# Performance work log

Hardware: AMD Instinct MI355X
Metric: run time of the kernel (lower is better)

## Reference

```python
import jax, jax.numpy as jnp
import numpy as np
import itertools

N_GRAPHS = 64
NODES_PER_GRAPH = 16
N_NODES = N_GRAPHS * NODES_PER_GRAPH  # 1024


def conv2d(x, w, b, stride=1):
    # x: [N, Cin, H, W], w: [Cout, Cin, 3, 3], padding=1 (same as torch Conv2d(...,3,stride,1))
    y = jax.lax.conv_general_dilated(
        x, w, (stride, stride), ((1, 1), (1, 1)),
        dimension_numbers=("NCHW", "OIHW", "NCHW"))
    return y + b[None, :, None, None]


def lrelu(x):
    return jax.nn.leaky_relu(x, 0.1)


def conv_mpn(x, edges, c1w, c1b, c2w, c2b, c3w, c3b):
    # ConvMPN: gather neighbour / non-neighbour node features, scatter_add to dst,
    # concat on channel dim, then 3 convs (no activation in between, as in source).
    n = x.shape[0]
    a, s, b = edges[:, 0], edges[:, 1], edges[:, 2]
    src = jnp.concatenate([a, b])  # bidirectional, matches torch cat([e0,e2]) / cat([e2,e0])
    dst = jnp.concatenate([b, a])
    pos = jnp.concatenate([s > 0, s > 0]).astype(x.dtype)
    neg = jnp.concatenate([s < 0, s < 0]).astype(x.dtype)
    gathered = x[src]  # [2E, C, H, W]
    neigh = jax.ops.segment_sum(gathered * pos[:, None, None, None], dst, num_segments=n)
    non = jax.ops.segment_sum(gathered * neg[:, None, None, None], dst, num_segments=n)
    h = jnp.concatenate([x, neigh, non], axis=1)  # [N, 3C, H, W]
    h = conv2d(h, c1w, c1b)
    h = conv2d(h, c2w, c2b)
    h = conv2d(h, c3w, c3b)
    return h


def setup_inputs() -> dict:
    key = jax.random.key(0)
    ks = iter(jax.random.split(key, 40))

    def p(shape):
        fan_in = int(np.prod(shape[1:])) if len(shape) > 1 else shape[0]
        return jax.random.normal(next(ks), shape, dtype=jnp.float32) / np.sqrt(fan_in)

    x = jax.random.normal(next(ks), (N_NODES, 32, 32), dtype=jnp.float32)
    t = jax.random.normal(next(ks), (N_NODES, 10), dtype=jnp.float32)

    # complete graph per sample; sign +/-1 marks neighbour vs non-neighbour
    pairs = np.array(list(itertools.combinations(range(NODES_PER_GRAPH), 2)))  # (120, 2)
    offs = np.arange(N_GRAPHS)[:, None] * NODES_PER_GRAPH
    aa = (pairs[None, :, 0] + offs).ravel()
    bb = (pairs[None, :, 1] + offs).ravel()
    rng = np.random.RandomState(0)
    sign = rng.choice(np.array([-1, 1]), size=aa.shape[0])
    edges = jnp.asarray(np.stack([aa, sign, bb], axis=1).astype(np.int64))
    nd_to_sample = jnp.asarray(np.repeat(np.arange(N_GRAPHS), NODES_PER_GRAPH).astype(np.int64))

    inp = {
        "x": x, "t": t, "edges": edges, "nd_to_sample": nd_to_sample,
        "w_t": p((8192, 10)), "b_t": jnp.zeros((8192,), jnp.float32),
        "c1w": p((16, 9, 3, 3)), "c1b": jnp.zeros((16,), jnp.float32),
        "c2w": p((16, 16, 3, 3)), "c2b": jnp.zeros((16,), jnp.float32),
        "c3w": p((16, 16, 3, 3)), "c3b": jnp.zeros((16,), jnp.float32),
        "m1c1w": p((32, 48, 3, 3)), "m1c1b": jnp.zeros((32,), jnp.float32),
        "m1c2w": p((32, 32, 3, 3)), "m1c2b": jnp.zeros((32,), jnp.float32),
        "m1c3w": p((16, 32, 3, 3)), "m1c3b": jnp.zeros((16,), jnp.float32),
        "ds1w": p((16, 16, 3, 3)), "ds1b": jnp.zeros((16,), jnp.float32),
        "m2c1w": p((32, 48, 3, 3)), "m2c1b": jnp.zeros((32,), jnp.float32),
        "m2c2w": p((32, 32, 3, 3)), "m2c2b": jnp.zeros((32,), jnp.float32),
        "m2c3w": p((16, 32, 3, 3)), "m2c3b": jnp.zeros((16,), jnp.float32),
        "ds2w": p((16, 16, 3, 3)), "ds2b": jnp.zeros((16,), jnp.float32),
        "d1w": p((256, 16, 3, 3)), "d1b": jnp.zeros((256,), jnp.float32),
        "d2w": p((128, 256, 3, 3)), "d2b": jnp.zeros((128,), jnp.float32),
        "d3w": p((128, 128, 3, 3)), "d3b": jnp.zeros((128,), jnp.float32),
        "pw": p((1, 128)), "pb": jnp.zeros((1,), jnp.float32),
    }
    return inp


def reference(x, t, edges, nd_to_sample,
              w_t, b_t, c1w, c1b, c2w, c2b, c3w, c3b,
              m1c1w, m1c1b, m1c2w, m1c2b, m1c3w, m1c3b, ds1w, ds1b,
              m2c1w, m2c1b, m2c2w, m2c2b, m2c3w, m2c3b, ds2w, ds2b,
              d1w, d1b, d2w, d2b, d3w, d3b, pw, pb):
    h = x.reshape(-1, 1, 32, 32)
    tt = (t @ w_t.T + b_t).reshape(-1, 8, 32, 32)
    h = jnp.concatenate([h, tt], axis=1)  # [N, 9, 32, 32]
    h = lrelu(conv2d(h, c1w, c1b))
    h = lrelu(conv2d(h, c2w, c2b))
    h = lrelu(conv2d(h, c3w, c3b))
    h = conv_mpn(h, edges, m1c1w, m1c1b, m1c2w, m1c2b, m1c3w, m1c3b)
    h = lrelu(conv2d(h, ds1w, ds1b, stride=2))  # 32 -> 16
    h = conv_mpn(h, edges, m2c1w, m2c1b, m2c2w, m2c2b, m2c3w, m2c3b)
    h = lrelu(conv2d(h, ds2w, ds2b, stride=2))  # 16 -> 8
    h = lrelu(conv2d(h, d1w, d1b, stride=2))    # 8 -> 4
    h = lrelu(conv2d(h, d2w, d2b, stride=2))    # 4 -> 2
    h = lrelu(conv2d(h, d3w, d3b, stride=2))    # 2 -> 1
    h = h.reshape(-1, h.shape[1])               # [N, 128]
    pooled = jax.ops.segment_sum(h, nd_to_sample, num_segments=N_GRAPHS)  # add_pool
    return pooled @ pw.T + pb                    # [B, 1]
```

## Files before the change

kernel.cpp:

```cpp
#include <hip/hip_runtime.h>
#include <hip/hip_bf16.h>


#define N_NODES   1024
#define N_GRAPHS  64

typedef __hip_bfloat16 bf16;
typedef __attribute__((ext_vector_type(8)))  short  short8;
typedef __attribute__((ext_vector_type(16))) float  f32x16;

__device__ __forceinline__ float bf2f(unsigned short s) {
    union { unsigned u; float f; } x; x.u = ((unsigned)s) << 16; return x.f;
}
__device__ __forceinline__ unsigned short f2bf(float f) {
    __hip_bfloat16 h = __float2bfloat16(f);
    return *reinterpret_cast<unsigned short*>(&h);
}
__device__ __forceinline__ uint4 pack8(const float* f) {
    uint4 r;
    r.x = f2bf(f[0]) | ((unsigned)f2bf(f[1]) << 16);
    r.y = f2bf(f[2]) | ((unsigned)f2bf(f[3]) << 16);
    r.z = f2bf(f[4]) | ((unsigned)f2bf(f[5]) << 16);
    r.w = f2bf(f[6]) | ((unsigned)f2bf(f[7]) << 16);
    return r;
}

template<int N>
__device__ __forceinline__ void zacc(f32x16* a) {
    #pragma unroll
    for (int i = 0; i < N; ++i)
        #pragma unroll
        for (int e = 0; e < 16; ++e) a[i][e] = 0.f;
}

template<int TPW, int NW>
__device__ __forceinline__ void mfma_rr32(
    const short* lds, int inbase, int zch,
    const unsigned short* wfb, int kkstride_sh,
    f32x16* acc, int wid, int lane)
{
    const int pxl = lane & 31, kg = lane >> 5;
    short8 wfr[9];
    #pragma unroll
    for (int kk = 0; kk < 9; ++kk)
        wfr[kk] = *(const short8*)(wfb + (size_t)kk * kkstride_sh + lane * 8);
    const int r0 = wid * TPW;
    #pragma unroll
    for (int ir = 0; ir < TPW + 2; ++ir) {
        int iy = r0 - 1 + ir;
        if (iy < 0 || iy > 31) continue;
        #pragma unroll
        for (int dx = 0; dx < 3; ++dx) {
            int ix = pxl + dx - 1;
            bool ok = (unsigned)ix < 32u;
            int chunk = ok ? (inbase + kg * 1024 + iy * 32 + ix) : zch;
            short8 B = *(const short8*)(lds + (size_t)chunk * 8);
            #pragma unroll
            for (int dy = -1; dy <= 1; ++dy) {
                constexpr int dummy = 0; (void)dummy;
                int a = ir - 1 - dy;
                if (a < 0 || a >= TPW) continue;
                acc[a] = __builtin_amdgcn_mfma_f32_32x32x16_bf16(
                    wfr[(dy + 1) * 3 + dx], B, acc[a], 0, 0, 0);
            }
        }
    }
}

template<int WIN, int WOUT, int STRIDE, int TPW, int TILES, int NW>
__device__ __forceinline__ void mfma_phase(
    const short* lds, int inbase, int zch,
    const unsigned short* wfb, int kkstride_sh,
    f32x16* acc, int wid, int lane)
{
    constexpr int NPI = WIN * WIN;
    const int pxl = lane & 31, kg = lane >> 5;
    short8 wfr[9];
    #pragma unroll
    for (int kk = 0; kk < 9; ++kk)
        wfr[kk] = *(const short8*)(wfb + (size_t)kk * kkstride_sh + lane * 8);
    #pragma unroll
    for (int t = 0; t < TPW; ++t) {
        int tile = wid * TPW + t;
        if (NW * TPW > TILES && tile >= TILES) continue;
        int oy, ox;
        if (WOUT == 32)      { oy = tile;                  ox = pxl;      }
        else if (WOUT == 16) { oy = tile * 2 + (pxl >> 4); ox = pxl & 15; }
        else                 { oy = tile * 4 + (pxl >> 3); ox = pxl & 7;  }
        #pragma unroll
        for (int kk = 0; kk < 9; ++kk) {
            int iy = STRIDE * oy + kk / 3 - 1, ix = STRIDE * ox + kk % 3 - 1;
            bool ok = ((unsigned)iy < (unsigned)WIN) && ((unsigned)ix < (unsigned)WIN);
            int chunk = ok ? (inbase + kg * NPI + iy * WIN + ix) : zch;
            acc[t] = __builtin_amdgcn_mfma_f32_32x32x16_bf16(
                wfr[kk], *(const short8*)(lds + (size_t)chunk * 8), acc[t], 0, 0, 0);
        }
    }
}

template<int WOUT, int COUT, int RELU, int TPW, int TILES, int NW, bool TOGLOBAL>
__device__ __forceinline__ void conv_epi(
    short* lds, int outbase, unsigned short* gout,
    const float* __restrict__ bias, const f32x16* acc, int wid, int lane)
{
    constexpr int NPO = WOUT * WOUT;
    const int pxl = lane & 31, kg = lane >> 5;
    #pragma unroll
    for (int t = 0; t < TPW; ++t) {
        int tile = wid * TPW + t;
        if (NW * TPW > TILES && tile >= TILES) continue;
        int oy, ox;
        if (WOUT == 32)      { oy = tile;                  ox = pxl;      }
        else if (WOUT == 16) { oy = tile * 2 + (pxl >> 4); ox = pxl & 15; }
        else                 { oy = tile * 4 + (pxl >> 3); ox = pxl & 7;  }
        int opx = oy * WOUT + ox;
        #pragma unroll
        for (int q = 0; q < COUT / 8; ++q) {
            unsigned short u[4];
            #pragma unroll
            for (int j = 0; j < 4; ++j) {
                int co = q * 8 + kg * 4 + j;
                float v = acc[t][4 * q + j] + bias[co];
                if (RELU) v = (v >= 0.f) ? v : 0.1f * v;
                u[j] = f2bf(v);
            }
            uint2 pk;
            pk.x = u[0] | ((unsigned)u[1] << 16);
            pk.y = u[2] | ((unsigned)u[3] << 16);
            if constexpr (TOGLOBAL)
                *(uint2*)(gout + ((size_t)q * NPO + opx) * 8 + kg * 4) = pk;
            else
                *(uint2*)(lds + ((size_t)(outbase + q * NPO + opx)) * 8 + kg * 4) = pk;
        }
    }
}

__global__ __launch_bounds__(64) void k_build_adj(
    const int* __restrict__ edges, int per_g,
    int* __restrict__ cnt, int* __restrict__ lst)
{
    int n = blockIdx.x * 64 + threadIdx.x;
    if (n >= N_NODES) return;
    int g = n >> 4;
    const int* eg = edges + (size_t)g * per_g * 3;
    int c = 0;
    for (int k = 0; k < per_g; ++k) {
        int a = eg[k * 3 + 0];
        int s = eg[k * 3 + 1];
        int b = eg[k * 3 + 2];
        int other = (a == n) ? b : ((b == n) ? a : -1);
        if (other >= 0 && (other >> 4) == g && c < 16) {
            lst[n * 16 + c] = other | ((s < 0) ? (int)0x80000000 : 0);
            ++c;
        }
    }
    cnt[n] = c;
}

#define N_PREP 14
struct PrepArgs {
    const float* w[N_PREP];
    unsigned short* o[N_PREP];
    int cin[N_PREP], cout[N_PREP], cig[N_PREP], mt[N_PREP], base[N_PREP];
};

__global__ __launch_bounds__(64) void k_prep_all(PrepArgs a)
{
    int b = blockIdx.x;
    int L = 0;
    #pragma unroll
    for (int i = 1; i < N_PREP; ++i) if (b >= a.base[i]) L = i;
    int rel = b - a.base[L];
    int MT = a.mt[L], CIG = a.cig[L];
    int m = rel % MT; rel /= MT;
    int cg = rel % CIG;
    int kk = rel / CIG;
    int Cin = a.cin[L], Cout = a.cout[L];
    int lane = threadIdx.x;
    int co = m * 32 + (lane & 31), kg = lane >> 5;
    float v[8];
    #pragma unroll
    for (int j = 0; j < 8; ++j) {
        int ci = cg * 16 + kg * 8 + j;
        v[j] = (co < Cout && ci < Cin) ? a.w[L][((size_t)co * Cin + ci) * 9 + kk] : 0.f;
    }
    *(uint4*)(a.o[L] + ((size_t)((kk * CIG + cg) * MT + m) * 64 + lane) * 8) = pack8(v);
}

__global__ __launch_bounds__(512) void k_front(
    const float* __restrict__ x, const float* __restrict__ t,
    const float* __restrict__ wt, const float* __restrict__ bt,
    const unsigned short* __restrict__ wf1, const float* __restrict__ b1,
    const unsigned short* __restrict__ wf2, const float* __restrict__ b2,
    const unsigned short* __restrict__ wf3, const float* __restrict__ b3,
    bf16* __restrict__ c3o, int node_base)
{
    __shared__ __align__(16) short lds[4097 * 8];
    __shared__ float s_t[10];
    const int nl = blockIdx.x, n = node_base + nl, tid = threadIdx.x;
    const int wid = tid >> 6, lane = tid & 63;
    if (tid < 10) s_t[tid] = t[n * 10 + tid];
    if (tid < 8)  lds[4096 * 8 + tid] = 0;
    __syncthreads();

    #pragma unroll
    for (int p = 0; p < 2; ++p) {
        int px = tid + p * 512;
        float ch[16];
        ch[0] = x[(size_t)n * 1024 + px];
        #pragma unroll
        for (int c = 1; c <= 8; ++c) {
            int o = (c - 1) * 1024 + px;
            float a = bt[o];
            const float* wr = wt + (size_t)o * 10;
            #pragma unroll
            for (int k = 0; k < 10; ++k) a += wr[k] * s_t[k];
            ch[c] = a;
        }
        #pragma unroll
        for (int c = 9; c < 16; ++c) ch[c] = 0.f;
        *(uint4*)(lds + (size_t)px * 8)          = pack8(ch);
        *(uint4*)(lds + (size_t)(1024 + px) * 8) = pack8(ch + 8);
    }
    __syncthreads();

    f32x16 acc[4];
    zacc<4>(acc);
    mfma_rr32<4, 8>(lds, 0, 4096, wf1, 512, acc, wid, lane);
    conv_epi<32, 16, 1, 4, 32, 8, false>(lds, 2048, nullptr, b1, acc, wid, lane);
    __syncthreads();
    zacc<4>(acc);
    mfma_rr32<4, 8>(lds, 2048, 4096, wf2, 512, acc, wid, lane);
    conv_epi<32, 16, 1, 4, 32, 8, false>(lds, 0, nullptr, b2, acc, wid, lane);
    __syncthreads();
    zacc<4>(acc);
    mfma_rr32<4, 8>(lds, 0, 4096, wf3, 512, acc, wid, lane);
    conv_epi<32, 16, 1, 4, 32, 8, true>(lds, 0,
        (unsigned short*)c3o + (size_t)nl * 16384, b3, acc, wid, lane);
}

__global__ __launch_bounds__(512) void k_mid1(
    const bf16* __restrict__ c3o, const bf16* __restrict__ g1p,
    const unsigned short* __restrict__ wf1, const float* __restrict__ b1,
    const unsigned short* __restrict__ wf2, const float* __restrict__ b2,
    const unsigned short* __restrict__ wf3, const float* __restrict__ b3,
    const unsigned short* __restrict__ wfd, const float* __restrict__ bd,
    bf16* __restrict__ ds1o)
{
    __shared__ __align__(16) short lds[8193 * 8];
    const int nl = blockIdx.x, tid = threadIdx.x;
    const int wid = tid >> 6, lane = tid & 63;
    if (tid < 8) lds[8192 * 8 + tid] = 0;

    uint4* l4 = (uint4*)lds;
    const uint4* s0 = (const uint4*)c3o + (size_t)nl * 2048;
    const uint4* s1 = (const uint4*)g1p + (size_t)nl * 4096;
    const uint4* s2 = s1 + 2048;
    #pragma unroll
    for (int r = 0; r < 4; ++r) l4[tid + r * 512] = s0[tid + r * 512];
    __syncthreads();

    f32x16 acc[4];
    zacc<4>(acc);
    uint4 pf[4];
    #pragma unroll
    for (int r = 0; r < 4; ++r) pf[r] = s1[tid + r * 512];
    mfma_rr32<4, 8>(lds, 0, 8192, wf1, 3 * 512, acc, wid, lane);
    #pragma unroll
    for (int r = 0; r < 4; ++r) l4[2048 + tid + r * 512] = pf[r];
    __syncthreads();
    #pragma unroll
    for (int r = 0; r < 4; ++r) pf[r] = s2[tid + r * 512];
    mfma_rr32<4, 8>(lds, 2048, 8192, wf1 + 512, 3 * 512, acc, wid, lane);
    #pragma unroll
    for (int r = 0; r < 4; ++r) l4[tid + r * 512] = pf[r];
    __syncthreads();
    mfma_rr32<4, 8>(lds, 0, 8192, wf1 + 1024, 3 * 512, acc, wid, lane);
    conv_epi<32, 32, 0, 4, 32, 8, false>(lds, 4096, nullptr, b1, acc, wid, lane);
    __syncthreads();

    zacc<4>(acc);
    mfma_rr32<4, 8>(lds, 4096, 8192, wf2,       2 * 512, acc, wid, lane);
    mfma_rr32<4, 8>(lds, 6144, 8192, wf2 + 512, 2 * 512, acc, wid, lane);
    conv_epi<32, 32, 0, 4, 32, 8, false>(lds, 0, nullptr, b2, acc, wid, lane);
    __syncthreads();

    zacc<4>(acc);
    mfma_rr32<4, 8>(lds, 0,    8192, wf3,       2 * 512, acc, wid, lane);
    mfma_rr32<4, 8>(lds, 2048, 8192, wf3 + 512, 2 * 512, acc, wid, lane);
    conv_epi<32, 16, 0, 4, 32, 8, false>(lds, 4096, nullptr, b3, acc, wid, lane);
    __syncthreads();

    zacc<1>(acc);
    mfma_phase<32, 16, 2, 1, 8, 8>(lds, 4096, 8192, wfd, 512, acc, wid, lane);
    conv_epi<16, 16, 1, 1, 8, 8, true>(lds, 0,
        (unsigned short*)ds1o + (size_t)nl * 4096, bd, acc, wid, lane);
}

__global__ __launch_bounds__(512) void k_mid2(
    const bf16* __restrict__ ds1o, const bf16* __restrict__ g2p,
    const unsigned short* __restrict__ wf1, const float* __restrict__ b1,
    const unsigned short* __restrict__ wf2, const float* __restrict__ b2,
    const unsigned short* __restrict__ wf3, const float* __restrict__ b3,
    const unsigned short* __restrict__ wfd, const float* __restrict__ bd,
    bf16* __restrict__ ds2o)
{
    __shared__ __align__(16) short lds[2049 * 8];
    const int nl = blockIdx.x, tid = threadIdx.x;
    const int wid = tid >> 6, lane = tid & 63;
    if (tid < 8) lds[2048 * 8 + tid] = 0;

    uint4* l4 = (uint4*)lds;
    const uint4* s0 = (const uint4*)ds1o + (size_t)nl * 512;
    const uint4* s1 = (const uint4*)g2p + (size_t)nl * 1024;
    const uint4* s2 = s1 + 512;
    l4[tid] = s0[tid];
    __syncthreads();

    f32x16 acc[1];
    zacc<1>(acc);
    uint4 pf;
    pf = s1[tid];
    mfma_phase<16, 16, 1, 1, 8, 8>(lds, 0, 2048, wf1, 3 * 512, acc, wid, lane);
    l4[512 + tid] = pf;
    __syncthreads();
    pf = s2[tid];
    mfma_phase<16, 16, 1, 1, 8, 8>(lds, 512, 2048, wf1 + 512, 3 * 512, acc, wid, lane);
    l4[tid] = pf;
    __syncthreads();
    mfma_phase<16, 16, 1, 1, 8, 8>(lds, 0, 2048, wf1 + 1024, 3 * 512, acc, wid, lane);
    conv_epi<16, 32, 0, 1, 8, 8, false>(lds, 1024, nullptr, b1, acc, wid, lane);
    __syncthreads();

    zacc<1>(acc);
    mfma_phase<16, 16, 1, 1, 8, 8>(lds, 1024, 2048, wf2,       2 * 512, acc, wid, lane);
    mfma_phase<16, 16, 1, 1, 8, 8>(lds, 1536, 2048, wf2 + 512, 2 * 512, acc, wid, lane);
    conv_epi<16, 32, 0, 1, 8, 8, false>(lds, 0, nullptr, b2, acc, wid, lane);
    __syncthreads();

    zacc<1>(acc);
    mfma_phase<16, 16, 1, 1, 8, 8>(lds, 0,   2048, wf3,       2 * 512, acc, wid, lane);
    mfma_phase<16, 16, 1, 1, 8, 8>(lds, 512, 2048, wf3 + 512, 2 * 512, acc, wid, lane);
    conv_epi<16, 16, 0, 1, 8, 8, false>(lds, 1024, nullptr, b3, acc, wid, lane);
    __syncthreads();

    zacc<1>(acc);
    mfma_phase<16, 8, 2, 1, 2, 8>(lds, 1024, 2048, wfd, 512, acc, wid, lane);
    conv_epi<8, 16, 1, 1, 2, 8, true>(lds, 0,
        (unsigned short*)ds2o + (size_t)nl * 1024, bd, acc, wid, lane);
}

template<int NPIX>
__global__ __launch_bounds__(256) void k_gather2(
    const bf16* __restrict__ in, const int* __restrict__ cnt,
    const int* __restrict__ lst, bf16* __restrict__ out, int node_base)
{
    constexpr int CPN = 2 * NPIX;
    __shared__ __align__(16) uint4 s_in[16 * 128];
    __shared__ int s_pos[16], s_neg[16];

    const int gl = blockIdx.x, sp = blockIdx.y, tid = threadIdx.x;
    const int gn0 = node_base + gl * 16, nl0 = gl * 16;

    if (tid < 16) {
        int c = cnt[gn0 + tid]; if (c > 16) c = 16;
        int pm = 0, nm = 0;
        for (int k = 0; k < c; ++k) {
            int e = lst[(size_t)(gn0 + tid) * 16 + k];
            int sl = (e & 0x7FFFFFFF) - gn0;
            if ((unsigned)sl < 16u) { if (e < 0) nm |= 1 << sl; else pm |= 1 << sl; }
        }
        s_pos[tid] = pm; s_neg[tid] = nm;
    }
    const uint4* in4 = (const uint4*)in;
    for (int i = tid; i < 2048; i += 256) {
        int srcn = i >> 7, chk = i & 127;
        s_in[i] = in4[(size_t)(nl0 + srcn) * CPN + sp * 128 + chk];
    }
    __syncthreads();

    const int dh = tid >> 7, ch = tid & 127;
    int pm[8], nm[8];
    #pragma unroll
    for (int dl = 0; dl < 8; ++dl) {
        pm[dl] = __builtin_amdgcn_readfirstlane(s_pos[dh * 8 + dl]);
        nm[dl] = __builtin_amdgcn_readfirstlane(s_neg[dh * 8 + dl]);
    }

    float aP[8][8], aN[8][8];
    #pragma unroll
    for (int dl = 0; dl < 8; ++dl)
        #pragma unroll
        for (int j = 0; j < 8; ++j) { aP[dl][j] = 0.f; aN[dl][j] = 0.f; }

    for (int s = 0; s < 16; ++s) {
        union { uint4 v; unsigned short u[8]; } q;
        q.v = s_in[s * 128 + ch];
        float f[8];
        #pragma unroll
        for (int j = 0; j < 8; ++j) f[j] = bf2f(q.u[j]);
        #pragma unroll
        for (int dl = 0; dl < 8; ++dl) {
            if ((pm[dl] >> s) & 1) {
                #pragma unroll
                for (int j = 0; j < 8; ++j) aP[dl][j] += f[j];
            }
            if ((nm[dl] >> s) & 1) {
                #pragma unroll
                for (int j = 0; j < 8; ++j) aN[dl][j] += f[j];
            }
        }
    }

    uint4* out4 = (uint4*)out;
    #pragma unroll
    for (int dl = 0; dl < 8; ++dl) {
        int d = nl0 + dh * 8 + dl;
        out4[((size_t)d * 2 + 0) * CPN + sp * 128 + ch] = pack8(aP[dl]);
        out4[((size_t)d * 2 + 1) * CPN + sp * 128 + ch] = pack8(aN[dl]);
    }
}

template<int HIN, int CIG, int COUT, int IPB, int FUSE_POOL>
__global__ __launch_bounds__(256) void k_tail(
    const bf16* __restrict__ in, const unsigned short* __restrict__ wf,
    const float* __restrict__ bias, bf16* __restrict__ out,
    const int* __restrict__ nd, const float* __restrict__ pw,
    float* __restrict__ pool_out, int nc, int node_base)
{
    constexpr int HOUT = HIN / 2, NPO = HOUT * HOUT, NPI = HIN * HIN;
    constexpr int MT  = (COUT + 31) / 32;
    constexpr int NT  = (IPB * NPO) / 32;
    constexpr int TOT = MT * NT;
    constexpr int TPW = TOT / 4;
    static_assert(TOT % 4 == 0, "tile count must divide over 4 waves");
    constexpr int CHUNKS = IPB * 2 * CIG * NPI;
    __shared__ __align__(16) short sbuf[CHUNKS * 8 + 8];

    const int tid = threadIdx.x, wid = tid >> 6, lane = tid & 63;
    const int col = lane & 31, kg = lane >> 5;
    const int img0 = blockIdx.x * IPB;

    {
        const uint4* src = (const uint4*)in + (size_t)img0 * (2 * CIG * NPI);
        uint4* dst = (uint4*)sbuf;
        int nav = nc - img0; if (nav > IPB) nav = IPB;
        int nch = nav * 2 * CIG * NPI;
        uint4 z = {0, 0, 0, 0};
        for (int i = tid; i < CHUNKS; i += 256) dst[i] = (i < nch) ? src[i] : z;
        if (tid < 8) sbuf[CHUNKS * 8 + tid] = 0;
    }
    __syncthreads();

    int imgb[TPW], poff[TPW][9];
    #pragma unroll
    for (int t = 0; t < TPW; ++t) {
        int tl = wid + 4 * t;
        int n  = tl % NT;
        int idx = n * 32 + col;
        int img = idx / NPO, px = idx % NPO;
        imgb[t] = img * (2 * CIG * NPI);
        int oy = px / HOUT, ox = px % HOUT;
        #pragma unroll
        for (int kk = 0; kk < 9; ++kk) {
            int iy = 2 * oy + kk / 3 - 1, ix = 2 * ox + kk % 3 - 1;
            bool ok = ((unsigned)iy < (unsigned)HIN) && ((unsigned)ix < (unsigned)HIN);
            poff[t][kk] = ok ? (iy * HIN + ix) : -1;
        }
    }

    f32x16 acc[TPW];
    #pragma unroll
    for (int t = 0; t < TPW; ++t)
        #pragma unroll
        for (int e = 0; e < 16; ++e) acc[t][e] = 0.f;

    for (int cig = 0; cig < CIG; ++cig) {
        #pragma unroll
        for (int t = 0; t < TPW; ++t) {
            int m = (wid + 4 * t) / NT;
            #pragma unroll
            for (int kk = 0; kk < 9; ++kk) {
                short8 wfr = *(const short8*)(wf +
                    ((size_t)((kk * CIG + cig) * MT + m) * 64 + lane) * 8);
                int chunk = (poff[t][kk] >= 0)
                          ? imgb[t] + (cig * 2 + kg) * NPI + poff[t][kk]
                          : CHUNKS;
                acc[t] = __builtin_amdgcn_mfma_f32_32x32x16_bf16(
                            wfr, *(const short8*)(sbuf + chunk * 8), acc[t], 0, 0, 0);
            }
        }
    }

    #pragma unroll
    for (int t = 0; t < TPW; ++t) {
        int tl = wid + 4 * t;
        int m = tl / NT, n = tl % NT;
        int idx = n * 32 + col;
        int img = idx / NPO, px = idx % NPO;
        bool live = (img0 + img) < nc;
        if (FUSE_POOL) {
            float part = 0.f;
            #pragma unroll
            for (int r = 0; r < 16; ++r) {
                int co = m * 32 + (r & 3) + 8 * (r >> 2) + 4 * kg;
                float v = acc[t][r] + bias[co];
                v = (v >= 0.f) ? v : 0.1f * v;
                part += v * pw[co];
            }
            part += __shfl_xor(part, 32, 64);
            if (kg == 0 && live) {
                int g = nd[node_base + img0 + img];
                if (g < 0) g = 0; if (g >= N_GRAPHS) g = N_GRAPHS - 1;
                atomicAdd(&pool_out[g], part);
            }
        } else if (live) {
            unsigned short* outp = (unsigned short*)out;
            #pragma unroll
            for (int q = 0; q < 4; ++q) {
                if (m * 32 + q * 8 < COUT) {
                    unsigned short u[4];
                    #pragma unroll
                    for (int j = 0; j < 4; ++j) {
                        int co = m * 32 + q * 8 + kg * 4 + j;
                        float v = acc[t][4 * q + j] + bias[co];
                        v = (v >= 0.f) ? v : 0.1f * v;
                        u[j] = f2bf(v);
                    }
                    uint2 pk;
                    pk.x = u[0] | ((unsigned)u[1] << 16);
                    pk.y = u[2] | ((unsigned)u[3] << 16);
                    *(uint2*)(outp + (((size_t)(img0 + img) * (COUT / 8)
                              + (m * 4 + q)) * NPO + px) * 8 + kg * 4) = pk;
                }
            }
        }
    }
}

__global__ void k_init_out(float* out, const float* __restrict__ pb)
{
    int i = threadIdx.x;
    if (i < N_GRAPHS) out[i] = pb[0];
}

extern "C" void kernel_launch(void* const* d_in, const int* in_sizes, int n_in,
                              void* d_out, int out_size, void* d_ws, size_t ws_size,
                              hipStream_t stream)
{
    const float* x     = (const float*)d_in[0];
    const float* t     = (const float*)d_in[1];
    const int*   edges = (const int*)d_in[2];
    const int*   nd    = (const int*)d_in[3];
    const float* w_t   = (const float*)d_in[4];
    const float* b_t   = (const float*)d_in[5];
    const float* c1w   = (const float*)d_in[6];
    const float* c1b   = (const float*)d_in[7];
    const float* c2w   = (const float*)d_in[8];
    const float* c2b   = (const float*)d_in[9];
    const float* c3w   = (const float*)d_in[10];
    const float* c3b   = (const float*)d_in[11];
    const float* m1c1w = (const float*)d_in[12];
    const float* m1c1b = (const float*)d_in[13];
    const float* m1c2w = (const float*)d_in[14];
    const float* m1c2b = (const float*)d_in[15];
    const float* m1c3w = (const float*)d_in[16];
    const float* m1c3b = (const float*)d_in[17];
    const float* ds1w  = (const float*)d_in[18];
    const float* ds1b  = (const float*)d_in[19];
    const float* m2c1w = (const float*)d_in[20];
    const float* m2c1b = (const float*)d_in[21];
    const float* m2c2w = (const float*)d_in[22];
    const float* m2c2b = (const float*)d_in[23];
    const float* m2c3w = (const float*)d_in[24];
    const float* m2c3b = (const float*)d_in[25];
    const float* ds2w  = (const float*)d_in[26];
    const float* ds2b  = (const float*)d_in[27];
    const float* d1w   = (const float*)d_in[28];
    const float* d1b   = (const float*)d_in[29];
    const float* d2w   = (const float*)d_in[30];
    const float* d2b   = (const float*)d_in[31];
    const float* d3w   = (const float*)d_in[32];
    const float* d3b   = (const float*)d_in[33];
    const float* pw    = (const float*)d_in[34];
    const float* pb    = (const float*)d_in[35];
    float* out = (float*)d_out;

    uint8_t* ws = (uint8_t*)d_ws;
    int* adj_cnt = (int*)ws;
    int* adj_lst = (int*)(ws + 4096);
    #define WF(i)  ((unsigned short*)(ws + (128u << 10) + (size_t)(i) * 32768))
    unsigned short* wt_ds1 = (unsigned short*)(ws + (416u  << 10));
    unsigned short* wt_ds2 = (unsigned short*)(ws + (428u  << 10));
    unsigned short* wt_d1  = (unsigned short*)(ws + (440u  << 10));
    unsigned short* wt_d2  = (unsigned short*)(ws + (512u  << 10));
    unsigned short* wt_d3  = (unsigned short*)(ws + (1088u << 10));

    const size_t RESV = 2ull << 20;
    size_t avail = (ws_size > RESV) ? ws_size - RESV : 0;
    int ncap = (int)(avail / (120 * 1024));
    ncap = (ncap / 16) * 16;
    if (ncap < 16) ncap = 16;
    if (ncap > N_NODES) ncap = N_NODES;
    uint8_t* R = ws + RESV;
    #define NB(off_kb) (R + (size_t)(off_kb) * 1024 * ncap)

    bf16*  c3o  = (bf16*)NB(0);
    bf16*  g1p  = (bf16*)NB(32);
    bf16*  ds1o = (bf16*)NB(96);
    bf16*  g2p  = (bf16*)NB(104);
    bf16*  ds2o = (bf16*)NB(0);
    bf16*  d1o  = (bf16*)NB(2);
    bf16*  d2o  = (bf16*)NB(10);

    int nE    = in_sizes[2] / 3;
    int per_g = nE / N_GRAPHS;

    k_build_adj<<<(N_NODES + 63) / 64, 64, 0, stream>>>(edges, per_g, adj_cnt, adj_lst);
    k_init_out<<<1, 64, 0, stream>>>(out, pb);

    {
        PrepArgs pa;
        const float* wsrc[N_PREP] = { c1w, c2w, c3w, m1c1w, m1c2w, m1c3w,
                                      m2c1w, m2c2w, m2c3w, ds1w, ds2w,
                                      d1w, d2w, d3w };
        unsigned short* wdst[N_PREP] = { WF(0), WF(1), WF(2), WF(3), WF(4), WF(5),
                                         WF(6), WF(7), WF(8), wt_ds1, wt_ds2,
                                         wt_d1, wt_d2, wt_d3 };
        int cin_[N_PREP]  = { 9, 16, 16, 48, 32, 32, 48, 32, 32, 16, 16, 16, 256, 128 };
        int cout_[N_PREP] = { 16, 16, 16, 32, 32, 16, 32, 32, 16, 16, 16, 256, 128, 128 };
        int cig_[N_PREP]  = { 1, 1, 1, 3, 2, 2, 3, 2, 2, 1, 1, 1, 16, 8 };
        int mt_[N_PREP]   = { 1, 1, 1, 1, 1, 1, 1, 1, 1, 1, 1, 8, 4, 4 };
        int total = 0;
        for (int i = 0; i < N_PREP; ++i) {
            pa.w[i] = wsrc[i]; pa.o[i] = wdst[i];
            pa.cin[i] = cin_[i]; pa.cout[i] = cout_[i];
            pa.cig[i] = cig_[i]; pa.mt[i] = mt_[i];
            pa.base[i] = total;
            total += 9 * cig_[i] * mt_[i];
        }
        k_prep_all<<<total, 64, 0, stream>>>(pa);
    }

    for (int nb = 0; nb < N_NODES; nb += ncap) {
        int nc = (N_NODES - nb < ncap) ? (N_NODES - nb) : ncap;
        int ng = nc / 16;

        k_front<<<nc, 512, 0, stream>>>(x, t, w_t, b_t,
            WF(0), c1b, WF(1), c2b, WF(2), c3b, c3o, nb);

        k_gather2<1024><<<dim3(ng, 16), 256, 0, stream>>>(c3o, adj_cnt, adj_lst, g1p, nb);

        k_mid1<<<nc, 512, 0, stream>>>(c3o, g1p,
            WF(3), m1c1b, WF(4), m1c2b, WF(5), m1c3b, wt_ds1, ds1b, ds1o);

        k_gather2<256><<<dim3(ng, 4), 256, 0, stream>>>(ds1o, adj_cnt, adj_lst, g2p, nb);

        k_mid2<<<nc, 512, 0, stream>>>(ds1o, g2p,
            WF(6), m2c1b, WF(7), m2c2b, WF(8), m2c3b, wt_ds2, ds2b, ds2o);

        k_tail<8, 1, 256, 4, 0><<<(nc + 3) / 4, 256, 0, stream>>>(
            ds2o, wt_d1, d1b, d1o, nullptr, nullptr, nullptr, nc, nb);
        k_tail<4, 16, 128, 8, 0><<<(nc + 7) / 8, 256, 0, stream>>>(
            d1o, wt_d2, d2b, d2o, nullptr, nullptr, nullptr, nc, nb);
        k_tail<2, 8, 128, 32, 1><<<(nc + 31) / 32, 256, 0, stream>>>(
            d2o, wt_d3, d3b, nullptr, nd, pw, out, nc, nb);
    }
    #undef NB
    #undef WF
}
```

Measured before the change: 285.3 us.

## Use async global-to-LDS loads, packed bf16 converts, and 1024-thread front/mid1 blocks

Replaces the register-staged global-to-LDS copies in k_mid1, k_mid2 and the gather kernel with the global_load_lds builtin, so data moves straight into shared memory without passing through VGPRs. Swaps the scalar bf16 conversions for the packed v_cvt_pk_bf16_f32 instruction. Doubles the block size of k_front and k_mid1 to 1024 threads, giving each wave 2 row tiles instead of 4. The larger blocks may raise register pressure and make barriers costlier. The async loads depend on correct barrier and wait ordering to be safe.

New measurement: 288.1 us. About the same (+1.0%).

```diff
diff --git a/kernel.cpp b/kernel.cpp
--- a/kernel.cpp
+++ b/kernel.cpp
@@ -12,17 +12,26 @@
 __device__ __forceinline__ float bf2f(unsigned short s) {
     union { unsigned u; float f; } x; x.u = ((unsigned)s) << 16; return x.f;
 }
-__device__ __forceinline__ unsigned short f2bf(float f) {
-    __hip_bfloat16 h = __float2bfloat16(f);
-    return *reinterpret_cast<unsigned short*>(&h);
+__device__ __forceinline__ unsigned cvtpk(float a, float b) {
+    unsigned r;
+    asm("v_cvt_pk_bf16_f32 %0, %1, %2" : "=v"(r) : "v"(a), "v"(b));
+    return r;
 }
 __device__ __forceinline__ uint4 pack8(const float* f) {
     uint4 r;
-    r.x = f2bf(f[0]) | ((unsigned)f2bf(f[1]) << 16);
-    r.y = f2bf(f[2]) | ((unsigned)f2bf(f[3]) << 16);
-    r.z = f2bf(f[4]) | ((unsigned)f2bf(f[5]) << 16);
-    r.w = f2bf(f[6]) | ((unsigned)f2bf(f[7]) << 16);
+    r.x = cvtpk(f[0], f[1]);
+    r.y = cvtpk(f[2], f[3]);
+    r.z = cvtpk(f[4], f[5]);
+    r.w = cvtpk(f[6], f[7]);
     return r;
+}
+__device__ __forceinline__ void gload16(const void* g, void* l) {
+    __builtin_amdgcn_global_load_lds(
+        reinterpret_cast<const __attribute__((address_space(1))) unsigned*>(
+            reinterpret_cast<uintptr_t>(g)),
+        reinterpret_cast<__attribute__((address_space(3))) unsigned*>(
+            reinterpret_cast<uintptr_t>(l)),
+        16, 0, 0);
 }
 
 template<int N>
@@ -57,7 +66,6 @@
             short8 B = *(const short8*)(lds + (size_t)chunk * 8);
             #pragma unroll
             for (int dy = -1; dy <= 1; ++dy) {
-                constexpr int dummy = 0; (void)dummy;
                 int a = ir - 1 - dy;
                 if (a < 0 || a >= TPW) continue;
                 acc[a] = __builtin_amdgcn_mfma_f32_32x32x16_bf16(
@@ -116,17 +124,16 @@
         int opx = oy * WOUT + ox;
         #pragma unroll
         for (int q = 0; q < COUT / 8; ++q) {
-            unsigned short u[4];
+            float v[4];
             #pragma unroll
             for (int j = 0; j < 4; ++j) {
                 int co = q * 8 + kg * 4 + j;
-                float v = acc[t][4 * q + j] + bias[co];
-                if (RELU) v = (v >= 0.f) ? v : 0.1f * v;
-                u[j] = f2bf(v);
+                float x = acc[t][4 * q + j] + bias[co];
+                v[j] = RELU ? ((x >= 0.f) ? x : 0.1f * x) : x;
             }
             uint2 pk;
-            pk.x = u[0] | ((unsigned)u[1] << 16);
-            pk.y = u[2] | ((unsigned)u[3] << 16);
+            pk.x = cvtpk(v[0], v[1]);
+            pk.y = cvtpk(v[2], v[3]);
             if constexpr (TOGLOBAL)
                 *(uint2*)(gout + ((size_t)q * NPO + opx) * 8 + kg * 4) = pk;
             else
@@ -187,7 +194,7 @@
     *(uint4*)(a.o[L] + ((size_t)((kk * CIG + cg) * MT + m) * 64 + lane) * 8) = pack8(v);
 }
 
-__global__ __launch_bounds__(512) void k_front(
+__global__ __launch_bounds__(1024) void k_front(
     const float* __restrict__ x, const float* __restrict__ t,
     const float* __restrict__ wt, const float* __restrict__ bt,
     const unsigned short* __restrict__ wf1, const float* __restrict__ b1,
@@ -203,9 +210,8 @@
     if (tid < 8)  lds[4096 * 8 + tid] = 0;
     __syncthreads();
 
-    #pragma unroll
-    for (int p = 0; p < 2; ++p) {
-        int px = tid + p * 512;
+    {
+        int px = tid;
         float ch[16];
         ch[0] = x[(size_t)n * 1024 + px];
         #pragma unroll
@@ -224,22 +230,22 @@
     }
     __syncthreads();
 
-    f32x16 acc[4];
-    zacc<4>(acc);
-    mfma_rr32<4, 8>(lds, 0, 4096, wf1, 512, acc, wid, lane);
-    conv_epi<32, 16, 1, 4, 32, 8, false>(lds, 2048, nullptr, b1, acc, wid, lane);
-    __syncthreads();
-    zacc<4>(acc);
-    mfma_rr32<4, 8>(lds, 2048, 4096, wf2, 512, acc, wid, lane);
-    conv_epi<32, 16, 1, 4, 32, 8, false>(lds, 0, nullptr, b2, acc, wid, lane);
-    __syncthreads();
-    zacc<4>(acc);
-    mfma_rr32<4, 8>(lds, 0, 4096, wf3, 512, acc, wid, lane);
-    conv_epi<32, 16, 1, 4, 32, 8, true>(lds, 0,
+    f32x16 acc[2];
+    zacc<2>(acc);
+    mfma_rr32<2, 16>(lds, 0, 4096, wf1, 512, acc, wid, lane);
+    conv_epi<32, 16, 1, 2, 32, 16, false>(lds, 2048, nullptr, b1, acc, wid, lane);
+    __syncthreads();
+    zacc<2>(acc);
+    mfma_rr32<2, 16>(lds, 2048, 4096, wf2, 512, acc, wid, lane);
+    conv_epi<32, 16, 1, 2, 32, 16, false>(lds, 0, nullptr, b2, acc, wid, lane);
+    __syncthreads();
+    zacc<2>(acc);
+    mfma_rr32<2, 16>(lds, 0, 4096, wf3, 512, acc, wid, lane);
+    conv_epi<32, 16, 1, 2, 32, 16, true>(lds, 0,
         (unsigned short*)c3o + (size_t)nl * 16384, b3, acc, wid, lane);
 }
 
-__global__ __launch_bounds__(512) void k_mid1(
+__global__ __launch_bounds__(1024) void k_mid1(
     const bf16* __restrict__ c3o, const bf16* __restrict__ g1p,
     const unsigned short* __restrict__ wf1, const float* __restrict__ b1,
     const unsigned short* __restrict__ wf2, const float* __restrict__ b2,
@@ -256,44 +262,39 @@
     const uint4* s0 = (const uint4*)c3o + (size_t)nl * 2048;
     const uint4* s1 = (const uint4*)g1p + (size_t)nl * 4096;
     const uint4* s2 = s1 + 2048;
-    #pragma unroll
-    for (int r = 0; r < 4; ++r) l4[tid + r * 512] = s0[tid + r * 512];
-    __syncthreads();
-
-    f32x16 acc[4];
-    zacc<4>(acc);
-    uint4 pf[4];
-    #pragma unroll
-    for (int r = 0; r < 4; ++r) pf[r] = s1[tid + r * 512];
-    mfma_rr32<4, 8>(lds, 0, 8192, wf1, 3 * 512, acc, wid, lane);
-    #pragma unroll
-    for (int r = 0; r < 4; ++r) l4[2048 + tid + r * 512] = pf[r];
-    __syncthreads();
-    #pragma unroll
-    for (int r = 0; r < 4; ++r) pf[r] = s2[tid + r * 512];
-    mfma_rr32<4, 8>(lds, 2048, 8192, wf1 + 512, 3 * 512, acc, wid, lane);
-    #pragma unroll
-    for (int r = 0; r < 4; ++r) l4[tid + r * 512] = pf[r];
-    __syncthreads();
-    mfma_rr32<4, 8>(lds, 0, 8192, wf1 + 1024, 3 * 512, acc, wid, lane);
-    conv_epi<32, 32, 0, 4, 32, 8, false>(lds, 4096, nullptr, b1, acc, wid, lane);
-    __syncthreads();
-
-    zacc<4>(acc);
-    mfma_rr32<4, 8>(lds, 4096, 8192, wf2,       2 * 512, acc, wid, lane);
-    mfma_rr32<4, 8>(lds, 6144, 8192, wf2 + 512, 2 * 512, acc, wid, lane);
-    conv_epi<32, 32, 0, 4, 32, 8, false>(lds, 0, nullptr, b2, acc, wid, lane);
-    __syncthreads();
-
-    zacc<4>(acc);
-    mfma_rr32<4, 8>(lds, 0,    8192, wf3,       2 * 512, acc, wid, lane);
-    mfma_rr32<4, 8>(lds, 2048, 8192, wf3 + 512, 2 * 512, acc, wid, lane);
-    conv_epi<32, 16, 0, 4, 32, 8, false>(lds, 4096, nullptr, b3, acc, wid, lane);
+    gload16(s0 + tid,        l4 + tid);
+    gload16(s0 + 1024 + tid, l4 + 1024 + tid);
+    gload16(s1 + tid,        l4 + 2048 + tid);
+    gload16(s1 + 1024 + tid, l4 + 3072 + tid);
+    __syncthreads();
+
+    f32x16 acc[2];
+    zacc<2>(acc);
+    mfma_rr32<2, 16>(lds, 0, 8192, wf1, 3 * 512, acc, wid, lane);
+    __syncthreads();
+    gload16(s2 + tid,        l4 + tid);
+    gload16(s2 + 1024 + tid, l4 + 1024 + tid);
+    mfma_rr32<2, 16>(lds, 2048, 8192, wf1 + 512, 3 * 512, acc, wid, lane);
+    __syncthreads();
+    mfma_rr32<2, 16>(lds, 0, 8192, wf1 + 1024, 3 * 512, acc, wid, lane);
+    conv_epi<32, 32, 0, 2, 32, 16, false>(lds, 4096, nullptr, b1, acc, wid, lane);
+    __syncthreads();
+
+    zacc<2>(acc);
+    mfma_rr32<2, 16>(lds, 4096, 8192, wf2,       2 * 512, acc, wid, lane);
+    mfma_rr32<2, 16>(lds, 6144, 8192, wf2 + 512, 2 * 512, acc, wid, lane);
+    conv_epi<32, 32, 0, 2, 32, 16, false>(lds, 0, nullptr, b2, acc, wid, lane);
+    __syncthreads();
+
+    zacc<2>(acc);
+    mfma_rr32<2, 16>(lds, 0,    8192, wf3,       2 * 512, acc, wid, lane);
+    mfma_rr32<2, 16>(lds, 2048, 8192, wf3 + 512, 2 * 512, acc, wid, lane);
+    conv_epi<32, 16, 0, 2, 32, 16, false>(lds, 4096, nullptr, b3, acc, wid, lane);
     __syncthreads();
 
     zacc<1>(acc);
-    mfma_phase<32, 16, 2, 1, 8, 8>(lds, 4096, 8192, wfd, 512, acc, wid, lane);
-    conv_epi<16, 16, 1, 1, 8, 8, true>(lds, 0,
+    mfma_phase<32, 16, 2, 1, 8, 16>(lds, 4096, 8192, wfd, 512, acc, wid, lane);
+    conv_epi<16, 16, 1, 1, 8, 16, true>(lds, 0,
         (unsigned short*)ds1o + (size_t)nl * 4096, bd, acc, wid, lane);
 }
 
@@ -314,19 +315,16 @@
     const uint4* s0 = (const uint4*)ds1o + (size_t)nl * 512;
     const uint4* s1 = (const uint4*)g2p + (size_t)nl * 1024;
     const uint4* s2 = s1 + 512;
-    l4[tid] = s0[tid];
+    gload16(s0 + tid, l4 + tid);
+    gload16(s1 + tid, l4 + 512 + tid);
     __syncthreads();
 
     f32x16 acc[1];
     zacc<1>(acc);
-    uint4 pf;
-    pf = s1[tid];
     mfma_phase<16, 16, 1, 1, 8, 8>(lds, 0, 2048, wf1, 3 * 512, acc, wid, lane);
-    l4[512 + tid] = pf;
-    __syncthreads();
-    pf = s2[tid];
+    __syncthreads();
+    gload16(s2 + tid, l4 + tid);
     mfma_phase<16, 16, 1, 1, 8, 8>(lds, 512, 2048, wf1 + 512, 3 * 512, acc, wid, lane);
-    l4[tid] = pf;
     __syncthreads();
     mfma_phase<16, 16, 1, 1, 8, 8>(lds, 0, 2048, wf1 + 1024, 3 * 512, acc, wid, lane);
     conv_epi<16, 32, 0, 1, 8, 8, false>(lds, 1024, nullptr, b1, acc, wid, lane);
@@ -373,9 +371,11 @@
         s_pos[tid] = pm; s_neg[tid] = nm;
     }
     const uint4* in4 = (const uint4*)in;
-    for (int i = tid; i < 2048; i += 256) {
+    #pragma unroll
+    for (int k = 0; k < 8; ++k) {
+        int i = tid + k * 256;
         int srcn = i >> 7, chk = i & 127;
-        s_in[i] = in4[(size_t)(nl0 + srcn) * CPN + sp * 128 + chk];
+        gload16(&in4[(size_t)(nl0 + srcn) * CPN + sp * 128 + chk], &s_in[i]);
     }
     __syncthreads();
 
@@ -519,17 +519,16 @@
             #pragma unroll
             for (int q = 0; q < 4; ++q) {
                 if (m * 32 + q * 8 < COUT) {
-                    unsigned short u[4];
+                    float v[4];
                     #pragma unroll
                     for (int j = 0; j < 4; ++j) {
                         int co = m * 32 + q * 8 + kg * 4 + j;
-                        float v = acc[t][4 * q + j] + bias[co];
-                        v = (v >= 0.f) ? v : 0.1f * v;
-                        u[j] = f2bf(v);
+                        float xx = acc[t][4 * q + j] + bias[co];
+                        v[j] = (xx >= 0.f) ? xx : 0.1f * xx;
                     }
                     uint2 pk;
-                    pk.x = u[0] | ((unsigned)u[1] << 16);
-                    pk.y = u[2] | ((unsigned)u[3] << 16);
+                    pk.x = cvtpk(v[0], v[1]);
+                    pk.y = cvtpk(v[2], v[3]);
                     *(uint2*)(outp + (((size_t)(img0 + img) * (COUT / 8)
                               + (m * 4 + q)) * NPO + px) * 8 + kg * 4) = pk;
                 }
@@ -646,12 +645,12 @@
         int nc = (N_NODES - nb < ncap) ? (N_NODES - nb) : ncap;
         int ng = nc / 16;
 
-        k_front<<<nc, 512, 0, stream>>>(x, t, w_t, b_t,
+        k_front<<<nc, 1024, 0, stream>>>(x, t, w_t, b_t,
             WF(0), c1b, WF(1), c2b, WF(2), c3b, c3o, nb);
 
         k_gather2<1024><<<dim3(ng, 16), 256, 0, stream>>>(c3o, adj_cnt, adj_lst, g1p, nb);
 
-        k_mid1<<<nc, 512, 0, stream>>>(c3o, g1p,
+        k_mid1<<<nc, 1024, 0, stream>>>(c3o, g1p,
             WF(3), m1c1b, WF(4), m1c2b, WF(5), m1c3b, wt_ds1, ds1b, ds1o);
 
         k_gather2<256><<<dim3(ng, 4), 256, 0, stream>>>(ds1o, adj_cnt, adj_lst, g2p, nb);
```
